# Kernel tuning notes

Measured on AMD Instinct MI355X. Metric: run time of the kernel, lower is better.

The kernel has to match this reference:

```python
import jax, jax.numpy as jnp
import numpy as np
from jax.scipy.special import logsumexp

B, T, V, C, H, D, SPW, NC = 16, 256, 10000, 4096, 256, 256, 32, 128


def _res(x, w1, b1, w2, b2):
    # ResLayer: x + relu(lin2(relu(lin1(x))))
    return x + jax.nn.relu(jax.nn.relu(x @ w1 + b1) @ w2 + b2)


def _log_phi(x, proj):
    # Performer-style log random features for the softmax kernel (smp param.)
    return x @ proj - 0.5 * jnp.sum(x * x, -1, keepdims=True)


def _log_matmul_exp(a, b):
    # logits[i,j] = logsumexp_d(a[i,d] + b[j,d]), stable, via a single GEMM
    ma = jnp.max(a, -1, keepdims=True)
    mb = jnp.max(b, -1, keepdims=True)
    return jnp.log(jnp.exp(a - ma) @ jnp.exp(b - mb).T) + ma + mb.T


def setup_inputs() -> dict:
    key = jax.random.key(0)
    ks = jax.random.split(key, 12)
    s = 1.0 / np.sqrt(H)  # xavier-ish scale
    inp = {
        "text": jax.random.randint(ks[0], (B, T), 0, V),
        "start_emb": jax.random.normal(ks[1], (H,), jnp.float32) * s,
        "start_w": jax.random.normal(ks[2], (5, H, H), jnp.float32) * s,
        "start_b": jnp.zeros((5, H), jnp.float32),
        "state_emb": jax.random.normal(ks[3], (C, H), jnp.float32) * s,
        "next_state_emb": jax.random.normal(ks[4], (C, H), jnp.float32) * s,
        "preterminal_emb": jax.random.normal(ks[5], (C, H), jnp.float32) * s,
        "terminal_w": jax.random.normal(ks[6], (4, H, H), jnp.float32) * s,
        "terminal_b": jnp.zeros((4, H), jnp.float32),
        "terminal_emb": jax.random.normal(ks[7], (V, H), jnp.float32) * s,
        "projection": jax.random.normal(ks[8], (H, D), jnp.float32),
    }
    # brown-cluster style assignment: each cluster owns SPW disjoint states
    w2c = jax.random.randint(ks[9], (V,), 0, NC)
    c2s = jnp.arange(NC)[:, None] * SPW + jnp.arange(SPW)[None, :]
    inp["word2state"] = c2s[w2c]  # [V, SPW]
    return inp


def reference(text, word2state, start_emb, start_w, start_b, state_emb,
              next_state_emb, preterminal_emb, terminal_w, terminal_b,
              terminal_emb, projection):
    # --- start distribution (tie_start=True uses next_state_emb) ---
    fx = start_emb @ start_w[0] + start_b[0]
    fx = _res(fx, start_w[1], start_b[1], start_w[2], start_b[2])
    fx = _res(fx, start_w[3], start_b[3], start_w[4], start_b[4])
    lpy = _log_phi(next_state_emb, projection)                      # [C, D]
    start_lp = jax.nn.log_softmax(
        _log_matmul_exp(_log_phi(fx[None], projection), lpy)[0])    # [C]
    # --- transition: kernelized low-rank logits, row log-softmax ---
    trans_lp = jax.nn.log_softmax(
        _log_matmul_exp(_log_phi(state_emb, projection), lpy), -1)  # [C, C]
    # --- emission: terminal_mlp + sparse word2state mask ---
    fp = _res(preterminal_emb, terminal_w[0], terminal_b[0], terminal_w[1], terminal_b[1])
    fp = _res(fp, terminal_w[2], terminal_b[2], terminal_w[3], terminal_b[3])
    emit_logits = _log_matmul_exp(_log_phi(fp, projection),
                                  _log_phi(terminal_emb, projection))  # [C, V]
    rows = word2state.reshape(-1)
    cols = jnp.repeat(jnp.arange(V), SPW)
    mask = jnp.zeros((C, V), bool).at[rows, cols].set(True)
    emit_lp = jax.nn.log_softmax(jnp.where(mask, emit_logits, -1e30), -1)
    # --- log-space forward algorithm over clamped sparse states ---
    clamped = word2state[text]                          # [B, T, SPW]
    emit_bt = emit_lp[clamped, text[:, :, None]]        # [B, T, SPW]
    alpha0 = start_lp[clamped[:, 0]] + emit_bt[:, 0]    # [B, SPW]
    xs = (jnp.swapaxes(clamped[:, :-1], 0, 1),
          jnp.swapaxes(clamped[:, 1:], 0, 1),
          jnp.swapaxes(emit_bt[:, 1:], 0, 1))

    def step(alpha, x):
        cp, cc, em = x                                   # [B,SPW] each / em [B,SPW]
        tr = trans_lp[cp[:, :, None], cc[:, None, :]]    # [B, SPW, SPW]
        return logsumexp(alpha[:, :, None] + tr, axis=1) + em, None

    alpha, _ = jax.lax.scan(step, alpha0, xs)
    return logsumexp(alpha, -1)                          # [B] log evidence
```

## Files before the change

### kernel.cpp

```cpp
#include <hip/hip_runtime.h>

#define B_   16
#define T_   256
#define V_   10000
#define C_   4096
#define H_   256
#define NC_  128
#define CAP_ 224
#define MST  33

typedef __bf16 bf16x8 __attribute__((ext_vector_type(8)));
typedef unsigned short u16x8 __attribute__((ext_vector_type(8)));
typedef float  f32x4  __attribute__((ext_vector_type(4)));

__device__ inline unsigned short f2bf(float f){
  unsigned int u = __float_as_uint(f);
  u += 0x7FFFu + ((u >> 16) & 1u);
  return (unsigned short)(u >> 16);
}
__device__ inline float bf2f(unsigned short u){
  return __uint_as_float(((unsigned int)u) << 16);
}
__device__ inline f32x4 mfma16(bf16x8 a, bf16x8 b, f32x4 c){
  return __builtin_amdgcn_mfma_f32_16x16x32_bf16(a, b, c, 0, 0, 0);
}
__device__ inline bf16x8 load_cvt8(const float* p){
  u16x8 u;
  #pragma unroll
  for (int i = 0; i < 8; ++i) u[i] = f2bf(p[i]);
  return __builtin_bit_cast(bf16x8, u);
}


__device__ inline void fx_accum(const float* __restrict__ W, const float* xh,
                                int j, float* __restrict__ Anext){
  int t = threadIdx.x;
  float p = 0.f;
  #pragma unroll
  for (int i = 0; i < 8; ++i)
    p = fmaf(xh[i], W[(size_t)(8*j + i)*256 + t], p);
  atomicAdd(&Anext[t], p);
}

__device__ inline void dev_mlp(const float* __restrict__ A,
    const unsigned short* __restrict__ Bt, const float* __restrict__ bias,
    const float* __restrict__ res, float* __restrict__ C, int r0)
{
  int tid = threadIdx.x;
  int w = tid >> 6, ln = tid & 63;
  int m16 = ln & 15, q = ln >> 4;
  int c0 = w*64;
  const float* a0 = A + (size_t)(r0 + m16)*256 + q*8;
  const float* a1 = a0 + 16*256;
  const unsigned short* bp0 = Bt + (size_t)(c0 + m16)*256 + q*8;
  f32x4 acc[2][4];
  #pragma unroll
  for (int i = 0; i < 2; ++i)
    #pragma unroll
    for (int jx = 0; jx < 4; ++jx) acc[i][jx] = (f32x4){0.f,0.f,0.f,0.f};
  #pragma unroll
  for (int kt = 0; kt < 8; ++kt){
    bf16x8 af0 = load_cvt8(a0 + kt*32);
    bf16x8 af1 = load_cvt8(a1 + kt*32);
    #pragma unroll
    for (int cj = 0; cj < 4; ++cj){
      bf16x8 bfj = *(const bf16x8*)(bp0 + (size_t)cj*16*256 + kt*32);
      acc[0][cj] = mfma16(af0, bfj, acc[0][cj]);
      acc[1][cj] = mfma16(af1, bfj, acc[1][cj]);
    }
  }
  #pragma unroll
  for (int ri = 0; ri < 2; ++ri){
    #pragma unroll
    for (int cj = 0; cj < 4; ++cj){
      #pragma unroll
      for (int r = 0; r < 4; ++r){
        int row = r0 + ri*16 + q*4 + r;
        int col = c0 + cj*16 + m16;
        float v = acc[ri][cj][r] + bias[col];
        v = fmaxf(v, 0.f);
        if (res) v += res[(size_t)row*256 + col];
        C[(size_t)row*256 + col] = v;
      }
    }
  }
}

__device__ inline void phi_core(const float* __restrict__ A,
    const unsigned short* __restrict__ Bt, int r0, int M, int w, int ln,
    f32x4 acc[2][4], float* lnrm)
{
  int m16 = ln & 15, q = ln >> 4;
  int c0 = w*64;
  int ra0 = r0 + m16;      if (ra0 > M-1) ra0 = M-1;
  int ra1 = r0 + 16 + m16; if (ra1 > M-1) ra1 = M-1;
  const float* a0 = A + (size_t)ra0*256 + q*8;
  const float* a1 = A + (size_t)ra1*256 + q*8;
  const unsigned short* bp0 = Bt + (size_t)(c0 + m16)*256 + q*8;
  float ss0 = 0.f, ss1 = 0.f;
  #pragma unroll
  for (int kt = 0; kt < 8; ++kt){
    float av0[8], av1[8];
    #pragma unroll
    for (int i2 = 0; i2 < 8; ++i2){ av0[i2] = a0[kt*32 + i2]; av1[i2] = a1[kt*32 + i2]; }
    u16x8 u0, u1;
    #pragma unroll
    for (int i2 = 0; i2 < 8; ++i2){
      u0[i2] = f2bf(av0[i2]); u1[i2] = f2bf(av1[i2]);
      ss0 = fmaf(av0[i2], av0[i2], ss0);
      ss1 = fmaf(av1[i2], av1[i2], ss1);
    }
    bf16x8 af0 = __builtin_bit_cast(bf16x8, u0);
    bf16x8 af1 = __builtin_bit_cast(bf16x8, u1);
    #pragma unroll
    for (int cj = 0; cj < 4; ++cj){
      bf16x8 bfj = *(const bf16x8*)(bp0 + (size_t)cj*16*256 + kt*32);
      acc[0][cj] = mfma16(af0, bfj, acc[0][cj]);
      acc[1][cj] = mfma16(af1, bfj, acc[1][cj]);
    }
  }
  ss0 += __shfl_xor(ss0, 16); ss0 += __shfl_xor(ss0, 32);
  ss1 += __shfl_xor(ss1, 16); ss1 += __shfl_xor(ss1, 32);
  if (w == 0 && q == 0){ lnrm[m16] = 0.5f*ss0; lnrm[16 + m16] = 0.5f*ss1; }
}

__device__ inline void dev_phiB(const float* __restrict__ A,
    const unsigned short* __restrict__ projT, unsigned short* __restrict__ Ebp,
    float* __restrict__ S, int r0, float* lnrm)
{
  int tid = threadIdx.x;
  int w = tid >> 6, ln = tid & 63;
  int m16 = ln & 15, q = ln >> 4;
  f32x4 acc[2][4];
  #pragma unroll
  for (int i = 0; i < 2; ++i)
    #pragma unroll
    for (int jx = 0; jx < 4; ++jx) acc[i][jx] = (f32x4){0.f,0.f,0.f,0.f};
  phi_core(A, projT, r0, C_, w, ln, acc, lnrm);
  __syncthreads();
  int c0 = w*64;
  #pragma unroll
  for (int cj = 0; cj < 4; ++cj){
    int col = c0 + cj*16 + m16;
    float cs = 0.f;
    #pragma unroll
    for (int ri = 0; ri < 2; ++ri){
      #pragma unroll
      for (int r = 0; r < 4; ++r){
        int row = ri*16 + q*4 + r;
        float e = __expf(acc[ri][cj][r] - lnrm[row]);
        Ebp[(size_t)(r0 + row)*256 + col] = f2bf(e);
        cs += e;
      }
    }
    cs += __shfl_xor(cs, 16); cs += __shfl_xor(cs, 32);
    if (q == 0) atomicAdd(&S[col], cs);
  }
}

__device__ inline void dev_phiA(const float* __restrict__ A,
    const unsigned short* __restrict__ projT, const float* __restrict__ S,
    unsigned short* __restrict__ Eap, int r0,
    float* lnrm, float* sS, float (*wrow)[32], float (*wden)[32])
{
  int tid = threadIdx.x;
  int w = tid >> 6, ln = tid & 63;
  int m16 = ln & 15, q = ln >> 4;
  sS[tid] = S[tid];
  f32x4 acc[2][4];
  #pragma unroll
  for (int i = 0; i < 2; ++i)
    #pragma unroll
    for (int jx = 0; jx < 4; ++jx) acc[i][jx] = (f32x4){0.f,0.f,0.f,0.f};
  phi_core(A, projT, r0, C_, w, ln, acc, lnrm);
  __syncthreads();
  int c0 = w*64;
  #pragma unroll
  for (int ri = 0; ri < 2; ++ri){
    #pragma unroll
    for (int r = 0; r < 4; ++r){
      int row = ri*16 + q*4 + r;
      float mv = -1e30f;
      #pragma unroll
      for (int cj = 0; cj < 4; ++cj){
        acc[ri][cj][r] -= lnrm[row];
        mv = fmaxf(mv, acc[ri][cj][r]);
      }
      #pragma unroll
      for (int d = 1; d < 16; d <<= 1) mv = fmaxf(mv, __shfl_xor(mv, d));
      if (m16 == 0) wrow[w][row] = mv;
    }
  }
  __syncthreads();
  float ev[2][4][4];
  float dsum[2][4];
  #pragma unroll
  for (int ri = 0; ri < 2; ++ri){
    #pragma unroll
    for (int r = 0; r < 4; ++r){
      int row = ri*16 + q*4 + r;
      float m = fmaxf(fmaxf(wrow[0][row], wrow[1][row]), fmaxf(wrow[2][row], wrow[3][row]));
      dsum[ri][r] = 0.f;
      #pragma unroll
      for (int cj = 0; cj < 4; ++cj){
        float scol = sS[c0 + cj*16 + m16];
        float e = __expf(acc[ri][cj][r] - m);
// ... 42 lines not shown
      }
      #pragma unroll
      for (int d = 1; d < 16; d <<= 1) mv = fmaxf(mv, __shfl_xor(mv, d));
      if (m16 == 0) wrow[w][row] = mv;
    }
  }
  __syncthreads();
  #pragma unroll
  for (int ri = 0; ri < 2; ++ri){
    #pragma unroll
    for (int r = 0; r < 4; ++r){
      int row = ri*16 + q*4 + r;
      int grow = r0 + row;
      float m = fmaxf(fmaxf(wrow[0][row], wrow[1][row]), fmaxf(wrow[2][row], wrow[3][row]));
      if (grow < M){
        #pragma unroll
        for (int cj = 0; cj < 4; ++cj){
          int col = c0 + cj*16 + m16;
          E[(size_t)grow*256 + col] = f2bf(__expf(acc[ri][cj][r] - m));
        }
        if (w == 0 && m16 == 0) mr[grow] = m;
      }
    }
  }
}

__device__ inline void dev_phiE(const float* __restrict__ A,
    const unsigned short* __restrict__ projT, unsigned short* __restrict__ E,
    float* __restrict__ mr, int M, int r0, float* lnrm, float (*wrow)[32])
{
  int tid = threadIdx.x;
  int w = tid >> 6, ln = tid & 63;
  f32x4 acc[2][4];
  #pragma unroll
  for (int i = 0; i < 2; ++i)
    #pragma unroll
    for (int jx = 0; jx < 4; ++jx) acc[i][jx] = (f32x4){0.f,0.f,0.f,0.f};
  phi_core(A, projT, r0, M, w, ln, acc, lnrm);
  __syncthreads();
  phiE_epilogue(acc, E, mr, M, r0, lnrm, wrow);
}

__global__ __launch_bounds__(256) void k_prep(
  const float* __restrict__ proj, const float* __restrict__ tw,
  unsigned short* __restrict__ projT, unsigned short* __restrict__ WT,
  const int* __restrict__ w2s, int* __restrict__ cnt, int* __restrict__ list,
  const float* __restrict__ se, const float* __restrict__ sw,
  float* __restrict__ Afx)
{
  int bx = blockIdx.x, tid = threadIdx.x;
  if (bx < 1280){
    int z = bx >> 8, dcol = bx & 255;
    const float* src = (z == 0) ? proj : (tw + (size_t)(z-1)*65536);
    unsigned short* dst = (z == 0) ? projT : (WT + (size_t)(z-1)*65536);
    dst[dcol*256 + tid] = f2bf(src[tid*256 + dcol]);
    return;
  }
  if (bx < 1320){
    int v = (bx - 1280)*256 + tid;
    if (v < V_){
      int k = w2s[v*32] >> 5;
      int pos = atomicAdd(&cnt[k], 1);
      if (pos < CAP_) list[k*CAP_ + pos] = v;
    }
    return;
  }
  int j = bx - 1320;
  float xh[8];
  #pragma unroll
  for (int i = 0; i < 8; ++i) xh[i] = se[8*j + i];
  fx_accum(sw, xh, j, Afx);
}

__global__ __launch_bounds__(256) void k_big1(
  const float* __restrict__ pre_emb, const unsigned short* __restrict__ WT,
  const float* __restrict__ term_b, float* __restrict__ H1,
  const float* __restrict__ next_emb, const unsigned short* __restrict__ projT,
  unsigned short* __restrict__ Ebp, float* __restrict__ S,
  const float* __restrict__ term_emb, unsigned short* __restrict__ Etb,
  float* __restrict__ mt,
  const float* __restrict__ sw, const float* __restrict__ sb,
  float* __restrict__ Afx)
{
  __shared__ float lnrm[32];
  __shared__ float wrow[4][32];
  int bx = blockIdx.x;
  if (bx < 128){
    dev_mlp(pre_emb, WT, term_b, nullptr, H1, bx*32);
  } else if (bx < 256){
    dev_phiB(next_emb, projT, Ebp, S, (bx - 128)*32, lnrm);
  } else if (bx < 569){
    dev_phiE(term_emb, projT, Etb, mt, V_, (bx - 256)*32, lnrm, wrow);
  } else {
    int j = bx - 569;
    float xh[8];
    #pragma unroll
    for (int i = 0; i < 8; ++i){ int h = 8*j + i; xh[i] = Afx[h] + sb[h]; }
    fx_accum(sw + 65536, xh, j, Afx + 256);
  }
}

__global__ __launch_bounds__(256) void k_big2(
  const float* __restrict__ H1, const unsigned short* __restrict__ WT,
  const float* __restrict__ term_b, const float* __restrict__ pre_emb,
  float* __restrict__ X2,
  const float* __restrict__ state_emb, const unsigned short* __restrict__ projT,
  const float* __restrict__ S, unsigned short* __restrict__ Eap,
  const float* __restrict__ sw, const float* __restrict__ sb,
  float* __restrict__ Afx)
{
  __shared__ float lnrm[32];
  __shared__ float sS[256];
  __shared__ float wrow[4][32];
  __shared__ float wden[4][32];
  int bx = blockIdx.x;
  if (bx < 128){
    dev_mlp(H1, WT + 1*65536, term_b + 256, pre_emb, X2, bx*32);
  } else if (bx < 256){
    dev_phiA(state_emb, projT, S, Eap, (bx - 128)*32, lnrm, sS, wrow, wden);
  } else {
    int j = bx - 256;
    float xh[8];
    #pragma unroll
    for (int i = 0; i < 8; ++i){ int h = 8*j + i; xh[i] = fmaxf(Afx[256 + h] + sb[256 + h], 0.f); }
    fx_accum(sw + 2*65536, xh, j, Afx + 512);
  }
}

__global__ __launch_bounds__(256) void k_mlpL2(
  const float* __restrict__ X2, const unsigned short* __restrict__ WT2,
  const float* __restrict__ bias, float* __restrict__ H1,
  const float* __restrict__ sw, const float* __restrict__ sb,
  float* __restrict__ Afx)
{
  int bx = blockIdx.x;
  if (bx < 128){
    dev_mlp(X2, WT2, bias, nullptr, H1, bx*32);
  } else {
    int j = bx - 128;
    float xh[8];
    #pragma unroll
    for (int i = 0; i < 8; ++i){
      int h = 8*j + i;
      float x0 = Afx[h] + sb[h];
      xh[i] = x0 + fmaxf(Afx[512 + h] + sb[512 + h], 0.f);
    }
    fx_accum(sw + 3*65536, xh, j, Afx + 768);
  }
}

__global__ __launch_bounds__(256) void k_mlp3phi(
  const float* __restrict__ H1, const unsigned short* __restrict__ WT3,
  const float* __restrict__ bias, const float* __restrict__ X2,
  const unsigned short* __restrict__ projT, unsigned short* __restrict__ Epb,
  float* __restrict__ mpp,
  const float* __restrict__ sw, const float* __restrict__ sb,
  float* __restrict__ Afx)
{
  __shared__ float sFP[32*257];
  __shared__ float lnrm[32];
  __shared__ float wrow[4][32];
  int bx = blockIdx.x;
  if (bx >= 128){
    int j = bx - 128;
    float xh[8];
    #pragma unroll
    for (int i = 0; i < 8; ++i){ int h = 8*j + i; xh[i] = fmaxf(Afx[768 + h] + sb[768 + h], 0.f); }
    fx_accum(sw + 4*65536, xh, j, Afx + 1024);
    return;
  }
  int r0 = bx*32;
  int tid = threadIdx.x;
  int w = tid >> 6, ln = tid & 63;
  int m16 = ln & 15, q = ln >> 4;
  int c0 = w*64;
  {
    const float* a0 = H1 + (size_t)(r0 + m16)*256 + q*8;
    const float* a1 = a0 + 16*256;
    const unsigned short* bp0 = WT3 + (size_t)(c0 + m16)*256 + q*8;
    f32x4 acc[2][4];
    #pragma unroll
    for (int i = 0; i < 2; ++i)
      #pragma unroll
      for (int jx = 0; jx < 4; ++jx) acc[i][jx] = (f32x4){0.f,0.f,0.f,0.f};
    #pragma unroll
    for (int kt = 0; kt < 8; ++kt){
      bf16x8 af0 = load_cvt8(a0 + kt*32);
      bf16x8 af1 = load_cvt8(a1 + kt*32);
      #pragma unroll
      for (int cj = 0; cj < 4; ++cj){
        bf16x8 bfj = *(const bf16x8*)(bp0 + (size_t)cj*16*256 + kt*32);
        acc[0][cj] = mfma16(af0, bfj, acc[0][cj]);
        acc[1][cj] = mfma16(af1, bfj, acc[1][cj]);
      }
    }
    #pragma unroll
    for (int ri = 0; ri < 2; ++ri){
      #pragma unroll
      for (int cj = 0; cj < 4; ++cj){
        #pragma unroll
        for (int r = 0; r < 4; ++r){
          int row = ri*16 + q*4 + r;
          int col = c0 + cj*16 + m16;
          float v = acc[ri][cj][r] + bias[col];
          v = fmaxf(v, 0.f);
          v += X2[(size_t)(r0 + row)*256 + col];
          sFP[row*257 + col] = v;
        }
      }
    }
  }
  __syncthreads();
  f32x4 acc[2][4];
  #pragma unroll
  for (int i = 0; i < 2; ++i)
    #pragma unroll
    for (int jx = 0; jx < 4; ++jx) acc[i][jx] = (f32x4){0.f,0.f,0.f,0.f};
  {
    const float* a0 = sFP + m16*257 + q*8;
    const float* a1 = sFP + (16 + m16)*257 + q*8;
    const unsigned short* bp0 = projT + (size_t)(c0 + m16)*256 + q*8;
    float ss0 = 0.f, ss1 = 0.f;
    #pragma unroll
    for (int kt = 0; kt < 8; ++kt){
      float av0[8], av1[8];
      #pragma unroll
      for (int i2 = 0; i2 < 8; ++i2){ av0[i2] = a0[kt*32 + i2]; av1[i2] = a1[kt*32 + i2]; }
      u16x8 u0, u1;
      #pragma unroll
      for (int i2 = 0; i2 < 8; ++i2){
        u0[i2] = f2bf(av0[i2]); u1[i2] = f2bf(av1[i2]);
        ss0 = fmaf(av0[i2], av0[i2], ss0);
        ss1 = fmaf(av1[i2], av1[i2], ss1);
      }
      bf16x8 af0 = __builtin_bit_cast(bf16x8, u0);
      bf16x8 af1 = __builtin_bit_cast(bf16x8, u1);
      #pragma unroll
      for (int cj = 0; cj < 4; ++cj){
        bf16x8 bfj = *(const bf16x8*)(bp0 + (size_t)cj*16*256 + kt*32);
        acc[0][cj] = mfma16(af0, bfj, acc[0][cj]);
        acc[1][cj] = mfma16(af1, bfj, acc[1][cj]);
      }
    }
    ss0 += __shfl_xor(ss0, 16); ss0 += __shfl_xor(ss0, 32);
    ss1 += __shfl_xor(ss1, 16); ss1 += __shfl_xor(ss1, 32);
    if (w == 0 && q == 0){ lnrm[m16] = 0.5f*ss0; lnrm[16 + m16] = 0.5f*ss1; }
  }
  __syncthreads();
  phiE_epilogue(acc, Epb, mpp, C_, r0, lnrm, wrow);
}

__global__ __launch_bounds__(256) void k_emit(
    const unsigned short* __restrict__ Epb, const float* __restrict__ mp,
    const unsigned short* __restrict__ Etb, const float* __restrict__ mt,
    const int* __restrict__ cnt, const int* __restrict__ list,
    float* __restrict__ emit_col,
    const float* __restrict__ proj, const float* __restrict__ sb,
    float* __restrict__ Afx)
{
  __shared__ float mtile[8][32];
  __shared__ float stile[8][32];
  __shared__ float mpl[32];
  __shared__ float denl[32];
  int k = blockIdx.x, tid = threadIdx.x;
  if (k >= 128){
    int j = k - 128;
    float xh[8];
    #pragma unroll
    for (int i = 0; i < 8; ++i){
      int h = 8*j + i;
      float x0 = Afx[h] + sb[h];
      float x2 = x0 + fmaxf(Afx[512 + h] + sb[512 + h], 0.f);
      xh[i] = x2 + fmaxf(Afx[1024 + h] + sb[1024 + h], 0.f);
    }
    fx_accum(proj, xh, j, Afx + 1280);
    return;
  }
  int w = tid >> 6, ln = tid & 63;
  int m16 = ln & 15, q = ln >> 4;
  if (tid < 32) mpl[tid] = mp[k*32 + tid];
  int n = cnt[k]; if (n > CAP_) n = CAP_;
  int nt = (n + 31) >> 5;
  const int* lp = list + k*CAP_;
  bf16x8 af0[8], af1[8];
  {
    const unsigned short* ap0 = Epb + (size_t)(k*32 + m16)*256 + q*8;
    const unsigned short* ap1 = ap0 + 16*256;
    #pragma unroll
    for (int kt = 0; kt < 8; ++kt){
      af0[kt] = *(const bf16x8*)(ap0 + kt*32);
      af1[kt] = *(const bf16x8*)(ap1 + kt*32);
    }
  }
  float lg[2][2][2][4];
  int   vj[2][2];
  #pragma unroll
  for (int u = 0; u < 2; ++u){
    int t = w + u*4;
    if (t >= nt) continue;
    int j0 = t*32 + m16, j1 = j0 + 16;
    int v0 = lp[(j0 < n) ? j0 : 0];
    int v1 = lp[(j1 < n) ? j1 : 0];
    vj[u][0] = v0; vj[u][1] = v1;
    float mt0 = (j0 < n) ? mt[v0] : 0.f;
    float mt1 = (j1 < n) ? mt[v1] : 0.f;
    const unsigned short* bp0 = Etb + (size_t)v0*256 + q*8;
    const unsigned short* bp1 = Etb + (size_t)v1*256 + q*8;
    f32x4 acc[2][2];
    #pragma unroll
    for (int mi = 0; mi < 2; ++mi)
      #pragma unroll
      for (int ni = 0; ni < 2; ++ni) acc[mi][ni] = (f32x4){0.f,0.f,0.f,0.f};
    #pragma unroll
// ... 109 lines not shown
  int m16 = ln & 15, q = ln >> 4;
  float mx = 0.f;
  #pragma unroll
  for (int mi = 0; mi < 2; ++mi)
    #pragma unroll
    for (int ni = 0; ni < 2; ++ni)
      #pragma unroll
      for (int r = 0; r < 4; ++r) mx = fmaxf(mx, acc[mi][ni][r]);
  #pragma unroll
  for (int d = 1; d < 64; d <<= 1) mx = fmaxf(mx, __shfl_xor(mx, d));
  float inv = 1.0f/mx;
  #pragma unroll
  for (int mi = 0; mi < 2; ++mi)
    #pragma unroll
    for (int ni = 0; ni < 2; ++ni)
      #pragma unroll
      for (int r = 0; r < 4; ++r)
        outp[(mi*16 + q*4 + r)*32 + ni*16 + m16] = f2bf(acc[mi][ni][r]*inv);
  if (ln == 0) *sOutG = sIn + __logf(mx);
}

__device__ inline void prod32(const float* L0, const float* L1, float* outp,
                              float sIn, float* sOut, int ln)
{
  f32x4 acc[2][2];
  #pragma unroll
  for (int mi = 0; mi < 2; ++mi)
    #pragma unroll
    for (int ni = 0; ni < 2; ++ni) acc[mi][ni] = (f32x4){0.f,0.f,0.f,0.f};
  prod_acc(L0, L1, acc, ln);
  wave_norm_store(acc, outp, sIn, sOut, ln);
}

__global__ __launch_bounds__(256) void k_chunk(
  const unsigned short* __restrict__ Eap, const unsigned short* __restrict__ Ebp,
  const float* __restrict__ emit_col, const int* __restrict__ text,
  const int* __restrict__ w2s, unsigned short* __restrict__ Gm, float* __restrict__ Gs)
{
  __shared__ float bufL[8][32*MST];
  __shared__ float bufN[4][32*MST];
  __shared__ float sL[8], sN[4], sT[2];
  int bc = blockIdx.x;
  int b = bc >> 5, ch = bc & 31;
  int tid = threadIdx.x;
  int w = tid >> 6, ln = tid & 63;
  int m16 = ln & 15, q = ln >> 4;
  #pragma unroll
  for (int u = 0; u < 2; ++u){
    int l = 2*w + u;
    int s = ch*8 + l;
    float* outp = bufL[l];
    if (s >= 255){
      for (int i = ln; i < 32*32; i += 64){
        int r = i >> 5, c = i & 31;
        outp[r*MST + c] = (r == c) ? 1.f : 0.f;
      }
      if (ln == 0) sL[l] = 0.f;
    } else {
      int vp = text[b*256 + s], vc = text[b*256 + s + 1];
      int bp = w2s[vp*32], bq = w2s[vc*32];
      const unsigned short* a0 = Eap + (size_t)(bp + m16)*256 + q*8;
      const unsigned short* b0 = Ebp + (size_t)(bq + m16)*256 + q*8;
      f32x4 acc[2][2];
      #pragma unroll
      for (int mi = 0; mi < 2; ++mi)
        #pragma unroll
        for (int ni = 0; ni < 2; ++ni) acc[mi][ni] = (f32x4){0.f,0.f,0.f,0.f};
      #pragma unroll
      for (int kt = 0; kt < 8; ++kt){
        bf16x8 a_0 = *(const bf16x8*)(a0 + kt*32);
        bf16x8 a_1 = *(const bf16x8*)(a0 + 16*256 + kt*32);
        bf16x8 b_0 = *(const bf16x8*)(b0 + kt*32);
        bf16x8 b_1 = *(const bf16x8*)(b0 + 16*256 + kt*32);
        acc[0][0] = mfma16(a_0, b_0, acc[0][0]);
        acc[0][1] = mfma16(a_0, b_1, acc[0][1]);
        acc[1][0] = mfma16(a_1, b_0, acc[1][0]);
        acc[1][1] = mfma16(a_1, b_1, acc[1][1]);
      }
      float e0 = __expf(emit_col[(size_t)vc*32 + m16]);
      float e1 = __expf(emit_col[(size_t)vc*32 + 16 + m16]);
      #pragma unroll
      for (int mi = 0; mi < 2; ++mi)
        #pragma unroll
        for (int r = 0; r < 4; ++r){
          acc[mi][0][r] *= e0;
          acc[mi][1][r] *= e1;
        }
      wave_norm_store(acc, outp, 0.f, &sL[l], ln);
    }
  }
  prod32(bufL[2*w], bufL[2*w+1], bufN[w], sL[2*w] + sL[2*w+1], &sN[w], ln);
  __syncthreads();
  if (w == 0){
    prod32(bufN[0], bufN[1], bufL[0], sN[0] + sN[1], &sT[0], ln);
    prod32(bufL[0], bufN[2], bufL[1], sT[0] + sN[2], &sT[1], ln);
    f32x4 acc[2][2];
    #pragma unroll
    for (int mi = 0; mi < 2; ++mi)
      #pragma unroll
      for (int ni = 0; ni < 2; ++ni) acc[mi][ni] = (f32x4){0.f,0.f,0.f,0.f};
    prod_acc(bufL[1], bufN[3], acc, ln);
    norm_store_g16(acc, Gm + (size_t)bc*1024, sT[1] + sN[3], Gs + bc, ln);
  }
}

__device__ inline void load_mat16(const unsigned short* __restrict__ g,
                                  float* __restrict__ d, int ln){
  #pragma unroll
  for (int p = 0; p < 16; ++p){
    int idx = p*64 + ln;
    int r = idx >> 5, c = idx & 31;
    d[r*MST + c] = bf2f(g[idx]);
  }
}

__global__ __launch_bounds__(512) void k_root(
  const unsigned short* __restrict__ Gm, const float* __restrict__ Gs,
  const float* __restrict__ Afx, const float* __restrict__ sb,
  const float* __restrict__ S,
  const unsigned short* __restrict__ Ebp, const float* __restrict__ emit_col,
  const int* __restrict__ text, const int* __restrict__ w2s, float* __restrict__ out)
{
  __shared__ float W[8][3][32*MST];
  __shared__ float sW[8], sT[1];
  __shared__ float eafx[256];
  __shared__ float red[4];
  int b = blockIdx.x;
  int tid = threadIdx.x;
  int w = tid >> 6, ln = tid & 63;
  float x4v = 0.f, pxv = 0.f;
  if (tid < 256){
    float x0 = Afx[tid] + sb[tid];
    float x2 = x0 + fmaxf(Afx[512 + tid] + sb[512 + tid], 0.f);
    x4v = x2 + fmaxf(Afx[1024 + tid] + sb[1024 + tid], 0.f);
    float v2 = x4v*x4v;
    #pragma unroll
    for (int d = 1; d < 64; d <<= 1) v2 += __shfl_xor(v2, d);
    if ((tid & 63) == 0) red[tid >> 6] = v2;
  }
  __syncthreads();
  float nx = red[0] + red[1] + red[2] + red[3];
  __syncthreads();
  if (tid < 256){
    pxv = Afx[1280 + tid] - 0.5f*nx;
    float m2 = pxv;
    #pragma unroll
    for (int d = 1; d < 64; d <<= 1) m2 = fmaxf(m2, __shfl_xor(m2, d));
    if ((tid & 63) == 0) red[tid >> 6] = m2;
  }
  __syncthreads();
  float m2g = fmaxf(fmaxf(red[0], red[1]), fmaxf(red[2], red[3]));
  if (tid < 256) eafx[tid] = __expf(pxv - m2g);
  __syncthreads();
  const unsigned short* G = Gm + ((size_t)(b*32 + w*4))*1024;
  const float* gs = Gs + b*32 + w*4;
  load_mat16(G,        W[w][0], ln);
  load_mat16(G + 1024, W[w][1], ln);
  prod32(W[w][0], W[w][1], W[w][2], gs[0] + gs[1], &sW[w], ln);
  load_mat16(G + 2048, W[w][0], ln);
  prod32(W[w][2], W[w][0], W[w][1], sW[w] + gs[2], &sW[w], ln);
  load_mat16(G + 3072, W[w][0], ln);
  prod32(W[w][1], W[w][0], W[w][2], sW[w] + gs[3], &sW[w], ln);
  __syncthreads();
  if (w == 0){
    float sAcc = sW[0];
    const float* cur = W[0][2];
    int dsel = 0;
    for (int j = 1; j < 8; ++j){
      float* dst = dsel ? W[0][1] : W[0][0];
      prod32(cur, W[j][2], dst, sAcc + sW[j], &sT[0], ln);
      sAcc = sT[0];
      cur = dst;
      dsel ^= 1;
    }
    float part = 0.f;
    for (int d = ln; d < 256; d += 64) part = fmaf(eafx[d], S[d], part);
    #pragma unroll
    for (int d2 = 1; d2 < 64; d2 <<= 1) part += __shfl_xor(part, d2);
    float dfx = part;
    int v0 = text[b*256];
    int k0 = w2s[v0*32];
    int j = ln & 31, h = ln >> 5;
    const unsigned short* er = Ebp + (size_t)(k0 + j)*256;
    float dot = 0.f;
    for (int d = h*128; d < h*128 + 128; ++d)
// ... 12 lines not shown
    #pragma unroll
    for (int d2 = 1; d2 < 32; d2 <<= 1) tot += __shfl_xor(tot, d2);
    if (ln == 0) out[b] = __logf(tot) + mz + sAcc - __logf(dfx);
  }
}

extern "C" void kernel_launch(void* const* d_in, const int* in_sizes, int n_in,
                              void* d_out, int out_size, void* d_ws, size_t ws_size,
                              hipStream_t stream)
{
  (void)in_sizes; (void)n_in; (void)out_size; (void)ws_size;
  const int*   text      = (const int*)  d_in[0];
  const float* start_emb = (const float*)d_in[1];
  const float* start_w   = (const float*)d_in[2];
  const float* start_b   = (const float*)d_in[3];
  const float* state_emb = (const float*)d_in[4];
  const float* next_emb  = (const float*)d_in[5];
  const float* pre_emb   = (const float*)d_in[6];
  const float* term_w    = (const float*)d_in[7];
  const float* term_b    = (const float*)d_in[8];
  const float* term_emb  = (const float*)d_in[9];
  const float* proj      = (const float*)d_in[10];
  const int*   w2s       = (const int*)  d_in[11];
  float* out = (float*)d_out;

  char* base = (char*)d_ws;
  size_t off = 0;
  auto alloc = [&](size_t bytes)->char*{
    char* p = base + off;
    off += (bytes + 255) & ~(size_t)255;
    return p;
  };
  int*   cnt = (int*)  alloc(128*4);
  float* Afx = (float*)alloc(6*256*4);
  float* S   = (float*)alloc(256*4);
  unsigned short* projT = (unsigned short*)alloc((size_t)65536*2);
  unsigned short* WT    = (unsigned short*)alloc((size_t)4*65536*2);
  float* H1   = (float*)alloc((size_t)C_*256*4);
  float* X2   = (float*)alloc((size_t)C_*256*4);
  unsigned short* Epb = (unsigned short*)alloc((size_t)C_*256*2);
  float* mpp  = (float*)alloc((size_t)C_*4);
  unsigned short* Etb = (unsigned short*)alloc((size_t)V_*256*2);
  float* mt   = (float*)alloc((size_t)V_*4);
  unsigned short* Eap = (unsigned short*)alloc((size_t)C_*256*2);
  unsigned short* Ebp = (unsigned short*)alloc((size_t)C_*256*2);
  int* list = (int*)alloc((size_t)128*CAP_*4);
  float* emit_col = (float*)alloc((size_t)V_*32*4);
  unsigned short* Gm = (unsigned short*)alloc((size_t)512*1024*2);
  float* Gs = (float*)alloc((size_t)512*4);

  (void)hipMemsetAsync(cnt, 0, 512 + 6144 + 1024, stream);

  k_prep<<<1352, 256, 0, stream>>>(proj, term_w, projT, WT, w2s, cnt, list,
                                   start_emb, start_w, Afx);
  k_big1<<<601, 256, 0, stream>>>(pre_emb, WT, term_b, H1,
                                  next_emb, projT, Ebp, S,
                                  term_emb, Etb, mt,
                                  start_w, start_b, Afx);
  k_big2<<<288, 256, 0, stream>>>(H1, WT, term_b, pre_emb, X2,
                                  state_emb, projT, S, Eap,
                                  start_w, start_b, Afx);
  k_mlpL2<<<160, 256, 0, stream>>>(X2, WT + 2*65536, term_b + 512, H1,
                                   start_w, start_b, Afx);
  k_mlp3phi<<<160, 256, 0, stream>>>(H1, WT + 3*65536, term_b + 768, X2,
                                     projT, Epb, mpp,
                                     start_w, start_b, Afx);
  k_emit<<<160, 256, 0, stream>>>(Epb, mpp, Etb, mt, cnt, list, emit_col,
                                  proj, start_b, Afx);
  k_chunk<<<512, 256, 0, stream>>>(Eap, Ebp, emit_col, text, w2s, Gm, Gs);
  k_root<<<16, 512, 0, stream>>>(Gm, Gs, Afx, start_b, S, Ebp, emit_col,
                                 text, w2s, out);
}
```

Measured before the change: 217.9 us.

## Fuse terminal MLP chain into one kernel and cut launches from eight to five

The four-layer preterminal MLP and its phi projection are fused into one block per 32-row tile. Intermediates stay in LDS (bf16 hidden, fp32 residual), so the H1/X2 global round trips and three kernel launches go away. The emit stage is merged into the phiA kernel. k_chunk now runs 512 threads, one transition matrix per wave, with a tree reduction. The last start-MLP layers and the projection are computed inside k_root instead of through atomic passes. The cost is a longer serial per-block chain in stageB, extra LDS pressure, and repeated small GEMV work in each root block.

Result: faster. 202.8 us (-6.9%).

```diff
diff --git a/kernel.cpp b/kernel.cpp
--- a/kernel.cpp
+++ b/kernel.cpp
@@ -8,6 +8,8 @@
 #define NC_  128
 #define CAP_ 224
 #define MST  33
+#define XST  257
+#define HST  264
 
 typedef __bf16 bf16x8 __attribute__((ext_vector_type(8)));
 typedef unsigned short u16x8 __attribute__((ext_vector_type(8)));
@@ -30,7 +32,12 @@
   for (int i = 0; i < 8; ++i) u[i] = f2bf(p[i]);
   return __builtin_bit_cast(bf16x8, u);
 }
-
+__device__ inline void zero_acc(f32x4 acc[2][4]){
+  #pragma unroll
+  for (int i = 0; i < 2; ++i)
+    #pragma unroll
+    for (int jx = 0; jx < 4; ++jx) acc[i][jx] = (f32x4){0.f,0.f,0.f,0.f};
+}
 
 __device__ inline void fx_accum(const float* __restrict__ W, const float* xh,
                                 int j, float* __restrict__ Anext){
@@ -42,22 +49,12 @@
   atomicAdd(&Anext[t], p);
 }
 
-__device__ inline void dev_mlp(const float* __restrict__ A,
-    const unsigned short* __restrict__ Bt, const float* __restrict__ bias,
-    const float* __restrict__ res, float* __restrict__ C, int r0)
-{
-  int tid = threadIdx.x;
-  int w = tid >> 6, ln = tid & 63;
-  int m16 = ln & 15, q = ln >> 4;
-  int c0 = w*64;
-  const float* a0 = A + (size_t)(r0 + m16)*256 + q*8;
+__device__ inline void mm_A_gf32(const float* __restrict__ A, size_t lda_row0,
+    const unsigned short* __restrict__ Bt, int w, int ln, f32x4 acc[2][4]){
+  int m16 = ln & 15, q = ln >> 4, c0 = w*64;
+  const float* a0 = A + lda_row0 + (size_t)m16*256 + q*8;
   const float* a1 = a0 + 16*256;
   const unsigned short* bp0 = Bt + (size_t)(c0 + m16)*256 + q*8;
-  f32x4 acc[2][4];
-  #pragma unroll
-  for (int i = 0; i < 2; ++i)
-    #pragma unroll
-    for (int jx = 0; jx < 4; ++jx) acc[i][jx] = (f32x4){0.f,0.f,0.f,0.f};
   #pragma unroll
   for (int kt = 0; kt < 8; ++kt){
     bf16x8 af0 = load_cvt8(a0 + kt*32);
@@ -69,20 +66,60 @@
       acc[1][cj] = mfma16(af1, bfj, acc[1][cj]);
     }
   }
-  #pragma unroll
-  for (int ri = 0; ri < 2; ++ri){
+}
+
+__device__ inline void mm_A_ldsbf(const unsigned short* sHb,
+    const unsigned short* __restrict__ Bt, int w, int ln, f32x4 acc[2][4]){
+  int m16 = ln & 15, q = ln >> 4, c0 = w*64;
+  const unsigned short* a0 = sHb + m16*HST + q*8;
+  const unsigned short* a1 = sHb + (16 + m16)*HST + q*8;
+  const unsigned short* bp0 = Bt + (size_t)(c0 + m16)*256 + q*8;
+  #pragma unroll
+  for (int kt = 0; kt < 8; ++kt){
+    bf16x8 af0 = *(const bf16x8*)(a0 + kt*32);
+    bf16x8 af1 = *(const bf16x8*)(a1 + kt*32);
     #pragma unroll
     for (int cj = 0; cj < 4; ++cj){
-      #pragma unroll
-      for (int r = 0; r < 4; ++r){
-        int row = r0 + ri*16 + q*4 + r;
-        int col = c0 + cj*16 + m16;
-        float v = acc[ri][cj][r] + bias[col];
-        v = fmaxf(v, 0.f);
-        if (res) v += res[(size_t)row*256 + col];
-        C[(size_t)row*256 + col] = v;
-      }
-    }
+      bf16x8 bfj = *(const bf16x8*)(bp0 + (size_t)cj*16*256 + kt*32);
+      acc[0][cj] = mfma16(af0, bfj, acc[0][cj]);
+      acc[1][cj] = mfma16(af1, bfj, acc[1][cj]);
+    }
+  }
+}
+
+__device__ inline void mm_A_ldsf32(const float* sX,
+    const unsigned short* __restrict__ Bt, int w, int ln, f32x4 acc[2][4],
+    float* lnrm){
+  int m16 = ln & 15, q = ln >> 4, c0 = w*64;
+  const float* a0 = sX + m16*XST + q*8;
+  const float* a1 = sX + (16 + m16)*XST + q*8;
+  const unsigned short* bp0 = Bt + (size_t)(c0 + m16)*256 + q*8;
+  float ss0 = 0.f, ss1 = 0.f;
+  #pragma unroll
+  for (int kt = 0; kt < 8; ++kt){
+    float av0[8], av1[8];
+    #pragma unroll
+    for (int i2 = 0; i2 < 8; ++i2){ av0[i2] = a0[kt*32 + i2]; av1[i2] = a1[kt*32 + i2]; }
+    u16x8 u0, u1;
+    #pragma unroll
+    for (int i2 = 0; i2 < 8; ++i2){
+      u0[i2] = f2bf(av0[i2]); u1[i2] = f2bf(av1[i2]);
+      ss0 = fmaf(av0[i2], av0[i2], ss0);
+      ss1 = fmaf(av1[i2], av1[i2], ss1);
+    }
+    bf16x8 af0 = __builtin_bit_cast(bf16x8, u0);
+    bf16x8 af1 = __builtin_bit_cast(bf16x8, u1);
+    #pragma unroll
+    for (int cj = 0; cj < 4; ++cj){
+      bf16x8 bfj = *(const bf16x8*)(bp0 + (size_t)cj*16*256 + kt*32);
+      acc[0][cj] = mfma16(af0, bfj, acc[0][cj]);
+      acc[1][cj] = mfma16(af1, bfj, acc[1][cj]);
+    }
+  }
+  if (lnrm){
+    ss0 += __shfl_xor(ss0, 16); ss0 += __shfl_xor(ss0, 32);
+    ss1 += __shfl_xor(ss1, 16); ss1 += __shfl_xor(ss1, 32);
+    if (w == 0 && q == 0){ lnrm[m16] = 0.5f*ss0; lnrm[16 + m16] = 0.5f*ss1; }
   }
 }
 
@@ -132,10 +169,7 @@
   int w = tid >> 6, ln = tid & 63;
   int m16 = ln & 15, q = ln >> 4;
   f32x4 acc[2][4];
-  #pragma unroll
-  for (int i = 0; i < 2; ++i)
-    #pragma unroll
-    for (int jx = 0; jx < 4; ++jx) acc[i][jx] = (f32x4){0.f,0.f,0.f,0.f};
+  zero_acc(acc);
   phi_core(A, projT, r0, C_, w, ln, acc, lnrm);
   __syncthreads();
   int c0 = w*64;
@@ -168,10 +202,7 @@
   int m16 = ln & 15, q = ln >> 4;
   sS[tid] = S[tid];
   f32x4 acc[2][4];
-  #pragma unroll
-  for (int i = 0; i < 2; ++i)
-    #pragma unroll
-    for (int jx = 0; jx < 4; ++jx) acc[i][jx] = (f32x4){0.f,0.f,0.f,0.f};
+  zero_acc(acc);
   phi_core(A, projT, r0, C_, w, ln, acc, lnrm);
   __syncthreads();
   int c0 = w*64;
@@ -280,10 +311,7 @@
   int tid = threadIdx.x;
   int w = tid >> 6, ln = tid & 63;
   f32x4 acc[2][4];
-  #pragma unroll
-  for (int i = 0; i < 2; ++i)
-    #pragma unroll
-    for (int jx = 0; jx < 4; ++jx) acc[i][jx] = (f32x4){0.f,0.f,0.f,0.f};
+  zero_acc(acc);
   phi_core(A, projT, r0, M, w, ln, acc, lnrm);
   __syncthreads();
   phiE_epilogue(acc, E, mr, M, r0, lnrm, wrow);
@@ -320,21 +348,83 @@
   fx_accum(sw, xh, j, Afx);
 }
 
-__global__ __launch_bounds__(256) void k_big1(
+__global__ __launch_bounds__(256) void k_stageB(
   const float* __restrict__ pre_emb, const unsigned short* __restrict__ WT,
-  const float* __restrict__ term_b, float* __restrict__ H1,
-  const float* __restrict__ next_emb, const unsigned short* __restrict__ projT,
-  unsigned short* __restrict__ Ebp, float* __restrict__ S,
+  const float* __restrict__ term_b,
+  const unsigned short* __restrict__ projT,
+  unsigned short* __restrict__ Epb, float* __restrict__ mpp,
+  const float* __restrict__ next_emb, unsigned short* __restrict__ Ebp,
+  float* __restrict__ S,
   const float* __restrict__ term_emb, unsigned short* __restrict__ Etb,
   float* __restrict__ mt,
   const float* __restrict__ sw, const float* __restrict__ sb,
   float* __restrict__ Afx)
 {
+  __shared__ __align__(16) float sX[32*XST];
+  __shared__ __align__(16) unsigned short sHb[32*HST];
   __shared__ float lnrm[32];
   __shared__ float wrow[4][32];
-  int bx = blockIdx.x;
+  int bx = blockIdx.x, tid = threadIdx.x;
+  int w = tid >> 6, ln = tid & 63;
+  int m16 = ln & 15, q = ln >> 4;
+  int c0 = w*64;
   if (bx < 128){
-    dev_mlp(pre_emb, WT, term_b, nullptr, H1, bx*32);
+    int r0 = bx*32;
+    f32x4 acc[2][4];
+    zero_acc(acc);
+    mm_A_gf32(pre_emb, (size_t)r0*256, WT, w, ln, acc);
+    #pragma unroll
+    for (int ri = 0; ri < 2; ++ri)
+      #pragma unroll
+      for (int cj = 0; cj < 4; ++cj)
+        #pragma unroll
+        for (int r = 0; r < 4; ++r){
+          int row = ri*16 + q*4 + r, col = c0 + cj*16 + m16;
+          sHb[row*HST + col] = f2bf(fmaxf(acc[ri][cj][r] + term_b[col], 0.f));
+        }
+    __syncthreads();
+    zero_acc(acc);
+    mm_A_ldsbf(sHb, WT + 65536, w, ln, acc);
+    #pragma unroll
+    for (int ri = 0; ri < 2; ++ri)
+      #pragma unroll
+      for (int cj = 0; cj < 4; ++cj)
+        #pragma unroll
+        for (int r = 0; r < 4; ++r){
+          int row = ri*16 + q*4 + r, col = c0 + cj*16 + m16;
+          float v = fmaxf(acc[ri][cj][r] + term_b[256 + col], 0.f);
+          sX[row*XST + col] = v + pre_emb[(size_t)(r0 + row)*256 + col];
+        }
+    __syncthreads();
+    zero_acc(acc);
+    mm_A_ldsf32(sX, WT + 2*65536, w, ln, acc, nullptr);
+    __syncthreads();
+    #pragma unroll
+    for (int ri = 0; ri < 2; ++ri)
+      #pragma unroll
+      for (int cj = 0; cj < 4; ++cj)
+        #pragma unroll
+        for (int r = 0; r < 4; ++r){
+          int row = ri*16 + q*4 + r, col = c0 + cj*16 + m16;
+          sHb[row*HST + col] = f2bf(fmaxf(acc[ri][cj][r] + term_b[512 + col], 0.f));
+        }
+    __syncthreads();
+    zero_acc(acc);
+    mm_A_ldsbf(sHb, WT + 3*65536, w, ln, acc);
+    #pragma unroll
+    for (int ri = 0; ri < 2; ++ri)
+      #pragma unroll
+      for (int cj = 0; cj < 4; ++cj)
+        #pragma unroll
+        for (int r = 0; r < 4; ++r){
+          int row = ri*16 + q*4 + r, col = c0 + cj*16 + m16;
+          sX[row*XST + col] += fmaxf(acc[ri][cj][r] + term_b[768 + col], 0.f);
+        }
+    __syncthreads();
+    zero_acc(acc);
+    mm_A_ldsf32(sX, projT, w, ln, acc, lnrm);
+    __syncthreads();
+    phiE_epilogue(acc, Epb, mpp, C_, r0, lnrm, wrow);
   } else if (bx < 256){
     dev_phiB(next_emb, projT, Ebp, S, (bx - 128)*32, lnrm);
   } else if (bx < 569){
@@ -348,12 +438,13 @@
   }
 }
 
-__global__ __launch_bounds__(256) void k_big2(
-  const float* __restrict__ H1, const unsigned short* __restrict__ WT,
-  const float* __restrict__ term_b, const float* __restrict__ pre_emb,
-  float* __restrict__ X2,
+__global__ __launch_bounds__(256) void k_stageC(
   const float* __restrict__ state_emb, const unsigned short* __restrict__ projT,
   const float* __restrict__ S, unsigned short* __restrict__ Eap,
+  const unsigned short* __restrict__ Epb, const float* __restrict__ mpp,
+  const unsigned short* __restrict__ Etb, const float* __restrict__ mt,
+  const int* __restrict__ cnt, const int* __restrict__ list,
+  float* __restrict__ emit_col,
   const float* __restrict__ sw, const float* __restrict__ sb,
   float* __restrict__ Afx)
 {
@@ -361,172 +452,27 @@
   __shared__ float sS[256];
   __shared__ float wrow[4][32];
   __shared__ float wden[4][32];
-  int bx = blockIdx.x;
-  if (bx < 128){
-    dev_mlp(H1, WT + 1*65536, term_b + 256, pre_emb, X2, bx*32);
-  } else if (bx < 256){
-    dev_phiA(state_emb, projT, S, Eap, (bx - 128)*32, lnrm, sS, wrow, wden);
-  } else {
-    int j = bx - 256;
-    float xh[8];
-    #pragma unroll
-    for (int i = 0; i < 8; ++i){ int h = 8*j + i; xh[i] = fmaxf(Afx[256 + h] + sb[256 + h], 0.f); }
-    fx_accum(sw + 2*65536, xh, j, Afx + 512);
-  }
-}
-
-__global__ __launch_bounds__(256) void k_mlpL2(
-  const float* __restrict__ X2, const unsigned short* __restrict__ WT2,
-  const float* __restrict__ bias, float* __restrict__ H1,
-  const float* __restrict__ sw, const float* __restrict__ sb,
-  float* __restrict__ Afx)
-{
-  int bx = blockIdx.x;
-  if (bx < 128){
-    dev_mlp(X2, WT2, bias, nullptr, H1, bx*32);
-  } else {
-    int j = bx - 128;
-    float xh[8];
-    #pragma unroll
-    for (int i = 0; i < 8; ++i){
-      int h = 8*j + i;
-      float x0 = Afx[h] + sb[h];
-      xh[i] = x0 + fmaxf(Afx[512 + h] + sb[512 + h], 0.f);
-    }
-    fx_accum(sw + 3*65536, xh, j, Afx + 768);
-  }
-}
-
-__global__ __launch_bounds__(256) void k_mlp3phi(
-  const float* __restrict__ H1, const unsigned short* __restrict__ WT3,
-  const float* __restrict__ bias, const float* __restrict__ X2,
-  const unsigned short* __restrict__ projT, unsigned short* __restrict__ Epb,
-  float* __restrict__ mpp,
-  const float* __restrict__ sw, const float* __restrict__ sb,
-  float* __restrict__ Afx)
-{
-  __shared__ float sFP[32*257];
-  __shared__ float lnrm[32];
-  __shared__ float wrow[4][32];
-  int bx = blockIdx.x;
-  if (bx >= 128){
-    int j = bx - 128;
-    float xh[8];
-    #pragma unroll
-    for (int i = 0; i < 8; ++i){ int h = 8*j + i; xh[i] = fmaxf(Afx[768 + h] + sb[768 + h], 0.f); }
-    fx_accum(sw + 4*65536, xh, j, Afx + 1024);
-    return;
-  }
-  int r0 = bx*32;
-  int tid = threadIdx.x;
-  int w = tid >> 6, ln = tid & 63;
-  int m16 = ln & 15, q = ln >> 4;
-  int c0 = w*64;
-  {
-    const float* a0 = H1 + (size_t)(r0 + m16)*256 + q*8;
-    const float* a1 = a0 + 16*256;
-    const unsigned short* bp0 = WT3 + (size_t)(c0 + m16)*256 + q*8;
-    f32x4 acc[2][4];
-    #pragma unroll
-    for (int i = 0; i < 2; ++i)
-      #pragma unroll
-      for (int jx = 0; jx < 4; ++jx) acc[i][jx] = (f32x4){0.f,0.f,0.f,0.f};
-    #pragma unroll
-    for (int kt = 0; kt < 8; ++kt){
-      bf16x8 af0 = load_cvt8(a0 + kt*32);
-      bf16x8 af1 = load_cvt8(a1 + kt*32);
-      #pragma unroll
-      for (int cj = 0; cj < 4; ++cj){
-        bf16x8 bfj = *(const bf16x8*)(bp0 + (size_t)cj*16*256 + kt*32);
-        acc[0][cj] = mfma16(af0, bfj, acc[0][cj]);
-        acc[1][cj] = mfma16(af1, bfj, acc[1][cj]);
-      }
-    }
-    #pragma unroll
-    for (int ri = 0; ri < 2; ++ri){
-      #pragma unroll
-      for (int cj = 0; cj < 4; ++cj){
-        #pragma unroll
-        for (int r = 0; r < 4; ++r){
-          int row = ri*16 + q*4 + r;
-          int col = c0 + cj*16 + m16;
-          float v = acc[ri][cj][r] + bias[col];
-          v = fmaxf(v, 0.f);
-          v += X2[(size_t)(r0 + row)*256 + col];
-          sFP[row*257 + col] = v;
-        }
-      }
-    }
-  }
-  __syncthreads();
-  f32x4 acc[2][4];
-  #pragma unroll
-  for (int i = 0; i < 2; ++i)
-    #pragma unroll
-    for (int jx = 0; jx < 4; ++jx) acc[i][jx] = (f32x4){0.f,0.f,0.f,0.f};
-  {
-    const float* a0 = sFP + m16*257 + q*8;
-    const float* a1 = sFP + (16 + m16)*257 + q*8;
-    const unsigned short* bp0 = projT + (size_t)(c0 + m16)*256 + q*8;
-    float ss0 = 0.f, ss1 = 0.f;
-    #pragma unroll
-    for (int kt = 0; kt < 8; ++kt){
-      float av0[8], av1[8];
-      #pragma unroll
-      for (int i2 = 0; i2 < 8; ++i2){ av0[i2] = a0[kt*32 + i2]; av1[i2] = a1[kt*32 + i2]; }
-      u16x8 u0, u1;
-      #pragma unroll
-      for (int i2 = 0; i2 < 8; ++i2){
-        u0[i2] = f2bf(av0[i2]); u1[i2] = f2bf(av1[i2]);
-        ss0 = fmaf(av0[i2], av0[i2], ss0);
-        ss1 = fmaf(av1[i2], av1[i2], ss1);
-      }
-      bf16x8 af0 = __builtin_bit_cast(bf16x8, u0);
-      bf16x8 af1 = __builtin_bit_cast(bf16x8, u1);
-      #pragma unroll
-      for (int cj = 0; cj < 4; ++cj){
-        bf16x8 bfj = *(const bf16x8*)(bp0 + (size_t)cj*16*256 + kt*32);
-        acc[0][cj] = mfma16(af0, bfj, acc[0][cj]);
-        acc[1][cj] = mfma16(af1, bfj, acc[1][cj]);
-      }
-    }
-    ss0 += __shfl_xor(ss0, 16); ss0 += __shfl_xor(ss0, 32);
-    ss1 += __shfl_xor(ss1, 16); ss1 += __shfl_xor(ss1, 32);
-    if (w == 0 && q == 0){ lnrm[m16] = 0.5f*ss0; lnrm[16 + m16] = 0.5f*ss1; }
-  }
-  __syncthreads();
-  phiE_epilogue(acc, Epb, mpp, C_, r0, lnrm, wrow);
-}
-
-__global__ __launch_bounds__(256) void k_emit(
-    const unsigned short* __restrict__ Epb, const float* __restrict__ mp,
-    const unsigned short* __restrict__ Etb, const float* __restrict__ mt,
-    const int* __restrict__ cnt, const int* __restrict__ list,
-    float* __restrict__ emit_col,
-    const float* __restrict__ proj, const float* __restrict__ sb,
-    float* __restrict__ Afx)
-{
   __shared__ float mtile[8][32];
   __shared__ float stile[8][32];
   __shared__ float mpl[32];
   __shared__ float denl[32];
-  int k = blockIdx.x, tid = threadIdx.x;
-  if (k >= 128){
-    int j = k - 128;
+  int bx = blockIdx.x, tid = threadIdx.x;
+  if (bx < 128){
+    dev_phiA(state_emb, projT, S, Eap, bx*32, lnrm, sS, wrow, wden);
+    return;
+  }
+  if (bx >= 256){
+    int j = bx - 256;
     float xh[8];
     #pragma unroll
-    for (int i = 0; i < 8; ++i){
-      int h = 8*j + i;
-      float x0 = Afx[h] + sb[h];
-      float x2 = x0 + fmaxf(Afx[512 + h] + sb[512 + h], 0.f);
-      xh[i] = x2 + fmaxf(Afx[1024 + h] + sb[1024 + h], 0.f);
-    }
-    fx_accum(proj, xh, j, Afx + 1280);
+    for (int i = 0; i < 8; ++i){ int h = 8*j + i; xh[i] = fmaxf(Afx[256 + h] + sb[256 + h], 0.f); }
+    fx_accum(sw + 2*65536, xh, j, Afx + 512);
     return;
   }
+  int k = bx - 128;
   int w = tid >> 6, ln = tid & 63;
   int m16 = ln & 15, q = ln >> 4;
-  if (tid < 32) mpl[tid] = mp[k*32 + tid];
+  if (tid < 32) mpl[tid] = mpp[k*32 + tid];
   int n = cnt[k]; if (n > CAP_) n = CAP_;
   int nt = (n + 31) >> 5;
   const int* lp = list + k*CAP_;
@@ -702,30 +648,44 @@
   wave_norm_store(acc, outp, sIn, sOut, ln);
 }
 
-__global__ __launch_bounds__(256) void k_chunk(
+__global__ __launch_bounds__(512) void k_chunk(
   const unsigned short* __restrict__ Eap, const unsigned short* __restrict__ Ebp,
   const float* __restrict__ emit_col, const int* __restrict__ text,
-  const int* __restrict__ w2s, unsigned short* __restrict__ Gm, float* __restrict__ Gs)
+  const int* __restrict__ w2s, unsigned short* __restrict__ Gm, float* __restrict__ Gs,
+  const float* __restrict__ sw, const float* __restrict__ sb,
+  float* __restrict__ Afx)
 {
   __shared__ float bufL[8][32*MST];
   __shared__ float bufN[4][32*MST];
-  __shared__ float sL[8], sN[4], sT[2];
-  int bc = blockIdx.x;
-  int b = bc >> 5, ch = bc & 31;
+  __shared__ float sL[8], sN[4];
+  int bx = blockIdx.x;
   int tid = threadIdx.x;
+  if (bx >= 512){
+    if (tid < 256){
+      int j = bx - 512;
+      float xh[8];
+      #pragma unroll
+      for (int i = 0; i < 8; ++i){
+        int h = 8*j + i;
+        float x0 = Afx[h] + sb[h];
+        xh[i] = x0 + fmaxf(Afx[512 + h] + sb[512 + h], 0.f);
+      }
+      fx_accum(sw + 3*65536, xh, j, Afx + 768);
+    }
+    return;
+  }
+  int b = bx >> 5, ch = bx & 31;
   int w = tid >> 6, ln = tid & 63;
   int m16 = ln & 15, q = ln >> 4;
-  #pragma unroll
-  for (int u = 0; u < 2; ++u){
-    int l = 2*w + u;
-    int s = ch*8 + l;
-    float* outp = bufL[l];
+  {
+    int s = ch*8 + w;
+    float* outp = bufL[w];
     if (s >= 255){
       for (int i = ln; i < 32*32; i += 64){
         int r = i >> 5, c = i & 31;
         outp[r*MST + c] = (r == c) ? 1.f : 0.f;
       }
-      if (ln == 0) sL[l] = 0.f;
+      if (ln == 0) sL[w] = 0.f;
     } else {
       int vp = text[b*256 + s], vc = text[b*256 + s + 1];
       int bp = w2s[vp*32], bq = w2s[vc*32];
@@ -756,21 +716,22 @@
           acc[mi][0][r] *= e0;
           acc[mi][1][r] *= e1;
         }
-      wave_norm_store(acc, outp, 0.f, &sL[l], ln);
-    }
-  }
-  prod32(bufL[2*w], bufL[2*w+1], bufN[w], sL[2*w] + sL[2*w+1], &sN[w], ln);
+      wave_norm_store(acc, outp, 0.f, &sL[w], ln);
+    }
+  }
+  __syncthreads();
+  if (w < 4) prod32(bufL[2*w], bufL[2*w+1], bufN[w], sL[2*w] + sL[2*w+1], &sN[w], ln);
+  __syncthreads();
+  if (w < 2) prod32(bufN[2*w], bufN[2*w+1], bufL[w], sN[2*w] + sN[2*w+1], &sL[w], ln);
   __syncthreads();
   if (w == 0){
-    prod32(bufN[0], bufN[1], bufL[0], sN[0] + sN[1], &sT[0], ln);
-    prod32(bufL[0], bufN[2], bufL[1], sT[0] + sN[2], &sT[1], ln);
     f32x4 acc[2][2];
     #pragma unroll
     for (int mi = 0; mi < 2; ++mi)
       #pragma unroll
       for (int ni = 0; ni < 2; ++ni) acc[mi][ni] = (f32x4){0.f,0.f,0.f,0.f};
-    prod_acc(bufL[1], bufN[3], acc, ln);
-    norm_store_g16(acc, Gm + (size_t)bc*1024, sT[1] + sN[3], Gs + bc, ln);
+    prod_acc(bufL[0], bufL[1], acc, ln);
+    norm_store_g16(acc, Gm + (size_t)bx*1024, sL[0] + sL[1], Gs + bx, ln);
   }
 }
 
@@ -787,40 +748,64 @@
 __global__ __launch_bounds__(512) void k_root(
   const unsigned short* __restrict__ Gm, const float* __restrict__ Gs,
   const float* __restrict__ Afx, const float* __restrict__ sb,
+  const float* __restrict__ sw, const float* __restrict__ proj,
   const float* __restrict__ S,
   const unsigned short* __restrict__ Ebp, const float* __restrict__ emit_col,
   const int* __restrict__ text, const int* __restrict__ w2s, float* __restrict__ out)
 {
   __shared__ float W[8][3][32*MST];
   __shared__ float sW[8], sT[1];
-  __shared__ float eafx[256];
+  __shared__ float eafx[256], sX2[256], sH[256];
+  __shared__ float gpart[2][256];
   __shared__ float red[4];
   int b = blockIdx.x;
   int tid = threadIdx.x;
   int w = tid >> 6, ln = tid & 63;
-  float x4v = 0.f, pxv = 0.f;
+  int t = tid & 255, u = tid >> 8;
   if (tid < 256){
     float x0 = Afx[tid] + sb[tid];
-    float x2 = x0 + fmaxf(Afx[512 + tid] + sb[512 + tid], 0.f);
-    x4v = x2 + fmaxf(Afx[1024 + tid] + sb[1024 + tid], 0.f);
-    float v2 = x4v*x4v;
+    sX2[tid] = x0 + fmaxf(Afx[512 + tid] + sb[512 + tid], 0.f);
+    sH[tid]  = fmaxf(Afx[768 + tid] + sb[768 + tid], 0.f);
+  }
+  __syncthreads();
+  {
+    float a = 0.f;
+    const float* Wp = sw + 4*65536 + (size_t)(128*u)*256 + t;
+    #pragma unroll 8
+    for (int h = 0; h < 128; ++h) a = fmaf(sH[128*u + h], Wp[(size_t)h*256], a);
+    gpart[u][t] = a;
+  }
+  __syncthreads();
+  if (tid < 256){
+    float A4 = gpart[0][t] + gpart[1][t];
+    float x4 = sX2[t] + fmaxf(A4 + sb[1024 + t], 0.f);
+    sX2[t] = x4;
+    float v2 = x4*x4;
     #pragma unroll
     for (int d = 1; d < 64; d <<= 1) v2 += __shfl_xor(v2, d);
-    if ((tid & 63) == 0) red[tid >> 6] = v2;
+    if ((t & 63) == 0) red[t >> 6] = v2;
   }
   __syncthreads();
   float nx = red[0] + red[1] + red[2] + red[3];
-  __syncthreads();
+  {
+    float a = 0.f;
+    const float* Pp = proj + (size_t)(128*u)*256 + t;
+    #pragma unroll 8
+    for (int h = 0; h < 128; ++h) a = fmaf(sX2[128*u + h], Pp[(size_t)h*256], a);
+    gpart[u][t] = a;
+  }
+  __syncthreads();
+  float pxv = 0.f;
   if (tid < 256){
-    pxv = Afx[1280 + tid] - 0.5f*nx;
+    pxv = gpart[0][t] + gpart[1][t] - 0.5f*nx;
     float m2 = pxv;
     #pragma unroll
     for (int d = 1; d < 64; d <<= 1) m2 = fmaxf(m2, __shfl_xor(m2, d));
-    if ((tid & 63) == 0) red[tid >> 6] = m2;
+    if ((t & 63) == 0) red[t >> 6] = m2;
   }
   __syncthreads();
   float m2g = fmaxf(fmaxf(red[0], red[1]), fmaxf(red[2], red[3]));
-  if (tid < 256) eafx[tid] = __expf(pxv - m2g);
+  if (tid < 256) eafx[t] = __expf(pxv - m2g);
   __syncthreads();
   const unsigned short* G = Gm + ((size_t)(b*32 + w*4))*1024;
   const float* gs = Gs + b*32 + w*4;
@@ -899,12 +884,10 @@
     return p;
   };
   int*   cnt = (int*)  alloc(128*4);
-  float* Afx = (float*)alloc(6*256*4);
+  float* Afx = (float*)alloc(4*256*4);
   float* S   = (float*)alloc(256*4);
   unsigned short* projT = (unsigned short*)alloc((size_t)65536*2);
   unsigned short* WT    = (unsigned short*)alloc((size_t)4*65536*2);
-  float* H1   = (float*)alloc((size_t)C_*256*4);
-  float* X2   = (float*)alloc((size_t)C_*256*4);
   unsigned short* Epb = (unsigned short*)alloc((size_t)C_*256*2);
   float* mpp  = (float*)alloc((size_t)C_*4);
   unsigned short* Etb = (unsigned short*)alloc((size_t)V_*256*2);
@@ -916,25 +899,18 @@
   unsigned short* Gm = (unsigned short*)alloc((size_t)512*1024*2);
   float* Gs = (float*)alloc((size_t)512*4);
 
-  (void)hipMemsetAsync(cnt, 0, 512 + 6144 + 1024, stream);
+  (void)hipMemsetAsync(cnt, 0, 512 + 4096 + 1024, stream);
 
   k_prep<<<1352, 256, 0, stream>>>(proj, term_w, projT, WT, w2s, cnt, list,
                                    start_emb, start_w, Afx);
-  k_big1<<<601, 256, 0, stream>>>(pre_emb, WT, term_b, H1,
-                                  next_emb, projT, Ebp, S,
-                                  term_emb, Etb, mt,
-                                  start_w, start_b, Afx);
-  k_big2<<<288, 256, 0, stream>>>(H1, WT, term_b, pre_emb, X2,
-                                  state_emb, projT, S, Eap,
-                                  start_w, start_b, Afx);
-  k_mlpL2<<<160, 256, 0, stream>>>(X2, WT + 2*65536, term_b + 512, H1,
+  k_stageB<<<601, 256, 0, stream>>>(pre_emb, WT, term_b, projT, Epb, mpp,
+                                    next_emb, Ebp, S, term_emb, Etb, mt,
+                                    start_w, start_b, Afx);
+  k_stageC<<<288, 256, 0, stream>>>(state_emb, projT, S, Eap,
+                                    Epb, mpp, Etb, mt, cnt, list, emit_col,
+                                    start_w, start_b, Afx);
+  k_chunk<<<544, 512, 0, stream>>>(Eap, Ebp, emit_col, text, w2s, Gm, Gs,
                                    start_w, start_b, Afx);
-  k_mlp3phi<<<160, 256, 0, stream>>>(H1, WT + 3*65536, term_b + 768, X2,
-                                     projT, Epb, mpp,
-                                     start_w, start_b, Afx);
-  k_emit<<<160, 256, 0, stream>>>(Epb, mpp, Etb, mt, cnt, list, emit_col,
-                                  proj, start_b, Afx);
-  k_chunk<<<512, 256, 0, stream>>>(Eap, Ebp, emit_col, text, w2s, Gm, Gs);
-  k_root<<<16, 512, 0, stream>>>(Gm, Gs, Afx, start_b, S, Ebp, emit_col,
-                                 text, w2s, out);
-}
+  k_root<<<16, 512, 0, stream>>>(Gm, Gs, Afx, start_b, start_w, proj, S,
+                                 Ebp, emit_col, text, w2s, out);
+}
```
